# Performance work log

Hardware: AMD Instinct MI355X
Metric: run time of the kernel (lower is better)

## Reference

```python
import jax, jax.numpy as jnp
import numpy as np

# PillarEncoder constants (KITTI PointPillars config)
VX, VY = 0.16, 0.16
PCR = (0.0, -39.68, -3.0, 69.12, 39.68, 1.0)
X_OFFSET = VX / 2 + PCR[0]          # 0.08
Y_OFFSET = VY / 2 + PCR[1]          # -39.60
X_GRID = int((PCR[3] - PCR[0]) / VX)  # 432
Y_GRID = int((PCR[4] - PCR[1]) / VY)  # 496
C_OUT = 64
BN_EPS = 1e-5


def _bn(x, g, b, m, v):
    # inference-mode BatchNorm over the last (channel) axis
    return (x - m) * (g / jnp.sqrt(v + BN_EPS)) + b


def setup_inputs() -> dict:
    key = jax.random.key(0)
    ks = jax.random.split(key, 8)
    B, PPB, N = 4, 16000, 32
    P = B * PPB  # 64000 pillars total
    pillars = jax.random.normal(ks[0], (P, N, 4), dtype=jnp.float32)
    # scale xyz into the point-cloud range roughly
    scale = jnp.array([20.0, 15.0, 1.0, 0.3], dtype=jnp.float32)
    shift = jnp.array([35.0, 0.0, -1.0, 0.5], dtype=jnp.float32)
    pillars = pillars * scale + shift
    bidx = jnp.repeat(jnp.arange(B, dtype=jnp.int64), PPB)
    xidx = jax.random.randint(ks[1], (P,), 0, X_GRID, dtype=jnp.int64)
    yidx = jax.random.randint(ks[2], (P,), 0, Y_GRID, dtype=jnp.int64)
    coors_batch = jnp.stack([bidx, xidx, yidx, jnp.zeros((P,), jnp.int64)], axis=1)
    npoints_per_pillar = jax.random.randint(ks[3], (P,), 1, N + 1, dtype=jnp.int64)
    W1 = jax.random.normal(ks[4], (C_OUT, 6), dtype=jnp.float32) * 0.3
    W2 = jax.random.normal(ks[5], (C_OUT, C_OUT), dtype=jnp.float32) * 0.1
    ones = jnp.ones((C_OUT,), jnp.float32)
    zeros = jnp.zeros((C_OUT,), jnp.float32)
    return {
        'pillars': pillars, 'coors_batch': coors_batch,
        'npoints_per_pillar': npoints_per_pillar, 'batch_size': 4,
        'W1': W1, 'g1': ones, 'b1': zeros, 'm1': zeros, 'v1': ones,
        'W2': W2, 'g2': ones, 'b2': zeros, 'm2': zeros, 'v2': ones,
    }


def reference(pillars, coors_batch, npoints_per_pillar, batch_size,
              W1, g1, b1, m1, v1, W2, g2, b2, m2, v2):
    P, N, _ = pillars.shape
    npf = npoints_per_pillar.astype(pillars.dtype)
    # offset from per-pillar point-cloud mean (xyz)
    center = jnp.sum(pillars[:, :, :3], axis=1, keepdims=True) / npf[:, None, None]
    offset_pt_center = pillars[:, :, :3] - center  # (P,N,3)
    # offset from pillar geometric center
    px = coors_batch[:, None, 1:2].astype(pillars.dtype) * VX + X_OFFSET
    py = coors_batch[:, None, 2:3].astype(pillars.dtype) * VY + Y_OFFSET
    x_off = pillars[:, :, 0:1] - px
    y_off = pillars[:, :, 1:2] - py
    features = jnp.concatenate(
        [pillars[:, :, 2:3], offset_pt_center, x_off, y_off], axis=-1)  # (P,N,6)
    # mask padded points
    mask = (jnp.arange(N)[None, :] < npoints_per_pillar[:, None])
    features = features * mask[:, :, None].astype(features.dtype)
    # pointwise MLP: Conv1d(k=1) == per-point linear; BN in inference mode
    h = jnp.einsum('pnc,oc->pno', features, W1)
    h = jax.nn.relu(_bn(h, g1, b1, m1, v1))
    h = jnp.einsum('pnc,oc->pno', h, W2)
    h = _bn(h, g2, b2, m2, v2)
    pooled = jnp.max(h, axis=1)  # (P, C_OUT)
    # matching torch advanced-index assignment)
    flat = (coors_batch[:, 0] * (X_GRID * Y_GRID)
            + coors_batch[:, 1] * Y_GRID + coors_batch[:, 2])
    canvas = jnp.zeros((batch_size * X_GRID * Y_GRID, C_OUT), pooled.dtype)
    canvas = canvas.at[flat].set(pooled)
    canvas = canvas.reshape(batch_size, X_GRID, Y_GRID, C_OUT)
    # torch: canvas.permute(2,1,0) -> (C, y_grid, x_grid); batched -> (B,C,Y,X)
    pseudo_image = jnp.transpose(canvas, (0, 3, 2, 1))
    return pseudo_image
```

## Files before the change

kernel.cpp:

```cpp
#include <hip/hip_runtime.h>
#include <math.h>

#define XG 432
#define YG 496
#define NPTS 32
#define COUT 64
#define ROWH 72
#define TILE 64

typedef __attribute__((ext_vector_type(8))) __bf16 bf16x8;
typedef __attribute__((ext_vector_type(16))) float f32x16;

union ABFrag { bf16x8 v; unsigned short s[8]; };

__device__ __forceinline__ unsigned short f2bf(float f) {
    unsigned u = __builtin_bit_cast(unsigned, f);
    u = (u + 0x7fffu + ((u >> 16) & 1u)) >> 16;
    return (unsigned short)u;
}

__global__ __launch_bounds__(256) void precompute_kernel(
    const float* __restrict__ W1,
    const float* __restrict__ g1, const float* __restrict__ b1,
    const float* __restrict__ m1, const float* __restrict__ v1,
    const float* __restrict__ W2,
    const float* __restrict__ g2, const float* __restrict__ b2,
    const float* __restrict__ m2, const float* __restrict__ v2,
    unsigned short* __restrict__ w1f,
    unsigned short* __restrict__ w2f,
    float* __restrict__ bnp)
{
    const int t = threadIdx.x;
    if (t < 128) {
        const int tt = t >> 6, lane = t & 63;
        const int half = lane >> 5, l31 = lane & 31;
        unsigned short vals[8] = {0,0,0,0,0,0,0,0};
        if (half == 0) {
            const int co = tt * 32 + l31;
            for (int k = 0; k < 6; ++k) vals[k] = f2bf(W1[co * 6 + k]);
        }
        for (int j = 0; j < 8; ++j) w1f[(tt * 64 + lane) * 8 + j] = vals[j];
    }
    if (t < 64) {
        const float s1 = g1[t] * rsqrtf(v1[t] + 1e-5f);
        bnp[t]       = s1;
        bnp[64 + t]  = b1[t] - m1[t] * s1;
        const float s2 = g2[t] * rsqrtf(v2[t] + 1e-5f);
        bnp[128 + t] = s2;
        bnp[192 + t] = b2[t] - m2[t] * s2;
    }
    for (int idx = t; idx < 512; idx += 256) {
        const int tt   = idx >> 8;
        const int kt   = (idx >> 6) & 3;
        const int lane = idx & 63;
        const int half = lane >> 5, l31 = lane & 31;
        const int co = tt * 32 + l31;
        for (int j = 0; j < 8; ++j) {
            const int kp = kt * 16 + half * 8 + j;
            const int ci = ((kp & 1) << 5) | (kp >> 1);
            w2f[((tt * 4 + kt) * 64 + lane) * 8 + j] = f2bf(W2[co * COUT + ci]);
        }
    }
}

__global__ __launch_bounds__(256) void pillar_mlp_kernel(
    const float* __restrict__ pillars,
    const int*   __restrict__ coors,
    const int*   __restrict__ npp,
    const unsigned short* __restrict__ w1f,
    const unsigned short* __restrict__ w2f,
    const float* __restrict__ bnp,
    float* __restrict__ pooled,
    int*   __restrict__ winner,
    int P)
{
    __shared__ unsigned int sh1[4][NPTS * (ROWH / 2)];

    const int w    = threadIdx.x >> 6;
    const int lane = threadIdx.x & 63;
    const int half = lane >> 5;
    const int l31  = lane & 31;
    const int p    = blockIdx.x * 4 + w;
    const int pc   = (p < P) ? p : (P - 1);

    const bf16x8* w2v = (const bf16x8*)w2f;
    bf16x8 b2f[8];
    #pragma unroll
    for (int i = 0; i < 8; ++i) b2f[i] = w2v[i * 64 + lane];
    const bf16x8* w1v = (const bf16x8*)w1f;
    const bf16x8 b1f0 = w1v[lane];
    const bf16x8 b1f1 = w1v[64 + lane];

    float s1a[2], bb1a[2], s2a[2], bb2a[2];
    #pragma unroll
    for (int t = 0; t < 2; ++t) {
        const int co = t * 32 + l31;
        s1a[t]  = bnp[co];
        bb1a[t] = bnp[64 + co];
        s2a[t]  = bnp[128 + co];
        bb2a[t] = bnp[192 + co];
    }

    float4 pt = make_float4(0.f, 0.f, 0.f, 0.f);
    if (lane < NPTS) pt = ((const float4*)pillars)[(size_t)pc * NPTS + lane];
    float sx = pt.x, sy = pt.y, sz = pt.z;
    #pragma unroll
    for (int m = 1; m <= 16; m <<= 1) {
        sx += __shfl_xor(sx, m);
        sy += __shfl_xor(sy, m);
        sz += __shfl_xor(sz, m);
    }
    const int   np     = npp[pc];
    const float inv_np = 1.0f / (float)np;
    const float cx = sx * inv_np, cy = sy * inv_np, cz = sz * inv_np;

    const int cb  = coors[pc * 4 + 0];
    const int cxg = coors[pc * 4 + 1];
    const int cyg = coors[pc * 4 + 2];
    const float px = (float)cxg * 0.16f + 0.08f;
    const float py = (float)cyg * 0.16f + (-39.60f);

    ABFrag a1;
    #pragma unroll
    for (int j = 0; j < 8; ++j) a1.s[j] = 0;
    if (lane < np) {
        a1.s[0] = f2bf(pt.z);
        a1.s[1] = f2bf(pt.x - cx);
        a1.s[2] = f2bf(pt.y - cy);
        a1.s[3] = f2bf(pt.z - cz);
        a1.s[4] = f2bf(pt.x - px);
        a1.s[5] = f2bf(pt.y - py);
    }

    f32x16 d0, d1;
    #pragma unroll
    for (int i = 0; i < 16; ++i) { d0[i] = 0.f; d1[i] = 0.f; }
    d0 = __builtin_amdgcn_mfma_f32_32x32x16_bf16(a1.v, b1f0, d0, 0, 0, 0);
    d1 = __builtin_amdgcn_mfma_f32_32x32x16_bf16(a1.v, b1f1, d1, 0, 0, 0);

    unsigned int* row = sh1[w];
    #pragma unroll
    for (int r = 0; r < 16; ++r) {
        const int point = (r & 3) + 8 * (r >> 2) + 4 * half;
        const float h0 = fmaxf(d0[r] * s1a[0] + bb1a[0], 0.f);
        const float h1 = fmaxf(d1[r] * s1a[1] + bb1a[1], 0.f);
        const unsigned pk = (unsigned)f2bf(h0) | ((unsigned)f2bf(h1) << 16);
        row[point * (ROWH / 2) + l31] = pk;
    }

    const unsigned short* rowh = (const unsigned short*)sh1[w];
    bf16x8 a2[4];
    #pragma unroll
    for (int kt = 0; kt < 4; ++kt)
        a2[kt] = *(const bf16x8*)(rowh + l31 * ROWH + kt * 16 + half * 8);

    f32x16 c0, c1;
    #pragma unroll
    for (int i = 0; i < 16; ++i) { c0[i] = 0.f; c1[i] = 0.f; }
    #pragma unroll
    for (int kt = 0; kt < 4; ++kt) {
        c0 = __builtin_amdgcn_mfma_f32_32x32x16_bf16(a2[kt], b2f[kt],     c0, 0, 0, 0);
        c1 = __builtin_amdgcn_mfma_f32_32x32x16_bf16(a2[kt], b2f[4 + kt], c1, 0, 0, 0);
    }

    float mx0 = -INFINITY, mx1 = -INFINITY;
    #pragma unroll
    for (int r = 0; r < 16; ++r) {
        mx0 = fmaxf(mx0, c0[r] * s2a[0] + bb2a[0]);
        mx1 = fmaxf(mx1, c1[r] * s2a[1] + bb2a[1]);
    }
    mx0 = fmaxf(mx0, __shfl_xor(mx0, 32));
    mx1 = fmaxf(mx1, __shfl_xor(mx1, 32));

    if (p < P) {
        pooled[(size_t)p * COUT + lane] = half ? mx1 : mx0;
        if (lane == 0)
            atomicMax(&winner[cb * (YG * XG) + cyg * XG + cxg], p);
    }
}

__global__ __launch_bounds__(256) void scatter_kernel(
    const float4* __restrict__ pooled4,
    const int*    __restrict__ winner,
    float4* __restrict__ out,
    int ntx)
{
    __shared__ int   swn[TILE];
    __shared__ float st[TILE * COUT];

    const int bid  = blockIdx.x;
    const int tx   = bid % ntx;
    const int rest = bid / ntx;
    const int y    = rest % YG;
    const int b    = rest / YG;
    const int x0   = tx * TILE;
    const int tid  = threadIdx.x;

    if (tid < TILE) {
        const int x = x0 + tid;
        swn[tid] = (x < XG) ? winner[(b * YG + y) * XG + x] : -1;
    }
    __syncthreads();

    float4* st4 = (float4*)st;
    #pragma unroll
    for (int i = 0; i < 4; ++i) {
        const int f    = i * 256 + tid;
        const int cell = f >> 4, q = f & 15;
        const int wn   = swn[cell];
        float4 v = make_float4(0.f, 0.f, 0.f, 0.f);
        if (wn >= 0) v = pooled4[(size_t)wn * 16 + q];
        const int qp = q ^ (((cell >> 2) ^ cell) & 15);
        st4[cell * 16 + qp] = v;
    }
    __syncthreads();

    #pragma unroll
    for (int i = 0; i < 4; ++i) {
        const int f   = i * 256 + tid;
        const int ch  = f >> 4, xi4 = f & 15;
        const int x   = x0 + xi4 * 4;
        if (x >= XG) continue;
        const int g = ch >> 2, cl = ch & 3;
        float vals[4];
        #pragma unroll
        for (int r = 0; r < 4; ++r) {
            const int cell = xi4 * 4 + r;
            const int gp = g ^ (((cell >> 2) ^ cell) & 15);
            vals[r] = st[cell * COUT + gp * 4 + cl];
        }
        out[((size_t)(b * COUT + ch) * YG + y) * (XG / 4) + (x >> 2)] =
            make_float4(vals[0], vals[1], vals[2], vals[3]);
    }
}

extern "C" void kernel_launch(void* const* d_in, const int* in_sizes, int n_in,
                              void* d_out, int out_size, void* d_ws, size_t ws_size,
                              hipStream_t stream) {
    const float* pillars = (const float*)d_in[0];
    const int*   coors   = (const int*)d_in[1];
    const int*   npp     = (const int*)d_in[2];
    const float* W1 = (const float*)d_in[4];
    const float* g1 = (const float*)d_in[5];
    const float* b1 = (const float*)d_in[6];
    const float* m1 = (const float*)d_in[7];
    const float* v1 = (const float*)d_in[8];
    const float* W2 = (const float*)d_in[9];
    const float* g2 = (const float*)d_in[10];
    const float* b2 = (const float*)d_in[11];
    const float* m2 = (const float*)d_in[12];
    const float* v2 = (const float*)d_in[13];

    const int P = in_sizes[2];
    const int B = out_size / (COUT * YG * XG);

    float* pooled = (float*)d_ws;
    int*   winner = (int*)((char*)d_ws + (size_t)COUT * P * sizeof(float));

    char* fragbase = (char*)d_out + (size_t)out_size * sizeof(float) - 11264;
    unsigned short* w1f = (unsigned short*)fragbase;
    unsigned short* w2f = (unsigned short*)(fragbase + 2048);
    float*          bnp = (float*)(fragbase + 10240);

    precompute_kernel<<<1, 256, 0, stream>>>(
        W1, g1, b1, m1, v1, W2, g2, b2, m2, v2, w1f, w2f, bnp);

    (void)hipMemsetAsync(winner, 0xFF, (size_t)B * YG * XG * sizeof(int), stream);

    pillar_mlp_kernel<<<(P + 3) / 4, 256, 0, stream>>>(
        pillars, coors, npp, w1f, w2f, bnp, pooled, winner, P);

    const int ntx = (XG + TILE - 1) / TILE;
    scatter_kernel<<<B * YG * ntx, 256, 0, stream>>>(
        (const float4*)pooled, winner, (float4*)d_out, ntx);
}
```

Before: 347.5 us.

## Fold BatchNorm into MLP weights, pack bf16 in hardware, use nontemporal output stores

The BN scales are folded into the bf16 W1/W2 fragments, and the BN1 bias rides along as a constant-one input column in the first MFMA. Only the BN2 bias is added, once, after the max-pool. This removes per-element scale/bias arithmetic from the MLP kernel. The ReLU output is packed with the hardware cvt_pk_bf16 instruction when available, and the scatter kernel writes the large pseudo-image with nontemporal stores to reduce cache pollution. Folding weights and bias into bf16 adds some rounding error compared with applying BN in fp32.

```diff
diff --git a/kernel.cpp b/kernel.cpp
--- a/kernel.cpp
+++ b/kernel.cpp
@@ -9,7 +9,9 @@
 #define TILE 64
 
 typedef __attribute__((ext_vector_type(8))) __bf16 bf16x8;
+typedef __attribute__((ext_vector_type(2))) __bf16 bf16x2;
 typedef __attribute__((ext_vector_type(16))) float f32x16;
+typedef __attribute__((ext_vector_type(4))) float f32x4;
 
 union ABFrag { bf16x8 v; unsigned short s[8]; };
 
@@ -17,6 +19,15 @@
     unsigned u = __builtin_bit_cast(unsigned, f);
     u = (u + 0x7fffu + ((u >> 16) & 1u)) >> 16;
     return (unsigned short)u;
+}
+
+__device__ __forceinline__ unsigned pack_bf16(float a, float b) {
+#if __has_builtin(__builtin_amdgcn_cvt_pk_bf16_f32)
+    bf16x2 r = __builtin_amdgcn_cvt_pk_bf16_f32(a, b);
+    return __builtin_bit_cast(unsigned, r);
+#else
+    return (unsigned)f2bf(a) | ((unsigned)f2bf(b) << 16);
+#endif
 }
 
 __global__ __launch_bounds__(256) void precompute_kernel(
@@ -28,7 +39,7 @@
     const float* __restrict__ m2, const float* __restrict__ v2,
     unsigned short* __restrict__ w1f,
     unsigned short* __restrict__ w2f,
-    float* __restrict__ bnp)
+    float* __restrict__ bb2v)
 {
     const int t = threadIdx.x;
     if (t < 128) {
@@ -37,17 +48,16 @@
         unsigned short vals[8] = {0,0,0,0,0,0,0,0};
         if (half == 0) {
             const int co = tt * 32 + l31;
-            for (int k = 0; k < 6; ++k) vals[k] = f2bf(W1[co * 6 + k]);
+            const float s1  = g1[co] * rsqrtf(v1[co] + 1e-5f);
+            const float bb1 = b1[co] - m1[co] * s1;
+            for (int k = 0; k < 6; ++k) vals[k] = f2bf(W1[co * 6 + k] * s1);
+            vals[6] = f2bf(bb1);
         }
         for (int j = 0; j < 8; ++j) w1f[(tt * 64 + lane) * 8 + j] = vals[j];
     }
     if (t < 64) {
-        const float s1 = g1[t] * rsqrtf(v1[t] + 1e-5f);
-        bnp[t]       = s1;
-        bnp[64 + t]  = b1[t] - m1[t] * s1;
         const float s2 = g2[t] * rsqrtf(v2[t] + 1e-5f);
-        bnp[128 + t] = s2;
-        bnp[192 + t] = b2[t] - m2[t] * s2;
+        bb2v[t] = b2[t] - m2[t] * s2;
     }
     for (int idx = t; idx < 512; idx += 256) {
         const int tt   = idx >> 8;
@@ -55,10 +65,11 @@
         const int lane = idx & 63;
         const int half = lane >> 5, l31 = lane & 31;
         const int co = tt * 32 + l31;
+        const float s2 = g2[co] * rsqrtf(v2[co] + 1e-5f);
         for (int j = 0; j < 8; ++j) {
             const int kp = kt * 16 + half * 8 + j;
             const int ci = ((kp & 1) << 5) | (kp >> 1);
-            w2f[((tt * 4 + kt) * 64 + lane) * 8 + j] = f2bf(W2[co * COUT + ci]);
+            w2f[((tt * 4 + kt) * 64 + lane) * 8 + j] = f2bf(W2[co * COUT + ci] * s2);
         }
     }
 }
@@ -69,7 +80,7 @@
     const int*   __restrict__ npp,
     const unsigned short* __restrict__ w1f,
     const unsigned short* __restrict__ w2f,
-    const float* __restrict__ bnp,
+    const float* __restrict__ bb2v,
     float* __restrict__ pooled,
     int*   __restrict__ winner,
     int P)
@@ -90,16 +101,7 @@
     const bf16x8* w1v = (const bf16x8*)w1f;
     const bf16x8 b1f0 = w1v[lane];
     const bf16x8 b1f1 = w1v[64 + lane];
-
-    float s1a[2], bb1a[2], s2a[2], bb2a[2];
-    #pragma unroll
-    for (int t = 0; t < 2; ++t) {
-        const int co = t * 32 + l31;
-        s1a[t]  = bnp[co];
-        bb1a[t] = bnp[64 + co];
-        s2a[t]  = bnp[128 + co];
-        bb2a[t] = bnp[192 + co];
-    }
+    const float bb2 = bb2v[lane];
 
     float4 pt = make_float4(0.f, 0.f, 0.f, 0.f);
     if (lane < NPTS) pt = ((const float4*)pillars)[(size_t)pc * NPTS + lane];
@@ -123,6 +125,7 @@
     ABFrag a1;
     #pragma unroll
     for (int j = 0; j < 8; ++j) a1.s[j] = 0;
+    if (half == 0) a1.s[6] = 0x3F80;
     if (lane < np) {
         a1.s[0] = f2bf(pt.z);
         a1.s[1] = f2bf(pt.x - cx);
@@ -142,10 +145,8 @@
     #pragma unroll
     for (int r = 0; r < 16; ++r) {
         const int point = (r & 3) + 8 * (r >> 2) + 4 * half;
-        const float h0 = fmaxf(d0[r] * s1a[0] + bb1a[0], 0.f);
-        const float h1 = fmaxf(d1[r] * s1a[1] + bb1a[1], 0.f);
-        const unsigned pk = (unsigned)f2bf(h0) | ((unsigned)f2bf(h1) << 16);
-        row[point * (ROWH / 2) + l31] = pk;
+        row[point * (ROWH / 2) + l31] =
+            pack_bf16(fmaxf(d0[r], 0.f), fmaxf(d1[r], 0.f));
     }
 
     const unsigned short* rowh = (const unsigned short*)sh1[w];
@@ -166,14 +167,14 @@
     float mx0 = -INFINITY, mx1 = -INFINITY;
     #pragma unroll
     for (int r = 0; r < 16; ++r) {
-        mx0 = fmaxf(mx0, c0[r] * s2a[0] + bb2a[0]);
-        mx1 = fmaxf(mx1, c1[r] * s2a[1] + bb2a[1]);
+        mx0 = fmaxf(mx0, c0[r]);
+        mx1 = fmaxf(mx1, c1[r]);
     }
     mx0 = fmaxf(mx0, __shfl_xor(mx0, 32));
     mx1 = fmaxf(mx1, __shfl_xor(mx1, 32));
 
     if (p < P) {
-        pooled[(size_t)p * COUT + lane] = half ? mx1 : mx0;
+        pooled[(size_t)p * COUT + lane] = (half ? mx1 : mx0) + bb2;
         if (lane == 0)
             atomicMax(&winner[cb * (YG * XG) + cyg * XG + cxg], p);
     }
@@ -182,7 +183,7 @@
 __global__ __launch_bounds__(256) void scatter_kernel(
     const float4* __restrict__ pooled4,
     const int*    __restrict__ winner,
-    float4* __restrict__ out,
+    f32x4* __restrict__ out,
     int ntx)
 {
     __shared__ int   swn[TILE];
@@ -222,15 +223,15 @@
         const int x   = x0 + xi4 * 4;
         if (x >= XG) continue;
         const int g = ch >> 2, cl = ch & 3;
-        float vals[4];
+        f32x4 vals;
         #pragma unroll
         for (int r = 0; r < 4; ++r) {
             const int cell = xi4 * 4 + r;
             const int gp = g ^ (((cell >> 2) ^ cell) & 15);
             vals[r] = st[cell * COUT + gp * 4 + cl];
         }
-        out[((size_t)(b * COUT + ch) * YG + y) * (XG / 4) + (x >> 2)] =
-            make_float4(vals[0], vals[1], vals[2], vals[3]);
+        __builtin_nontemporal_store(vals,
+            &out[((size_t)(b * COUT + ch) * YG + y) * (XG / 4) + (x >> 2)]);
     }
 }
 
@@ -258,19 +259,19 @@
     int*   winner = (int*)((char*)d_ws + (size_t)COUT * P * sizeof(float));
 
     char* fragbase = (char*)d_out + (size_t)out_size * sizeof(float) - 11264;
-    unsigned short* w1f = (unsigned short*)fragbase;
-    unsigned short* w2f = (unsigned short*)(fragbase + 2048);
-    float*          bnp = (float*)(fragbase + 10240);
+    unsigned short* w1f  = (unsigned short*)fragbase;
+    unsigned short* w2f  = (unsigned short*)(fragbase + 2048);
+    float*          bb2v = (float*)(fragbase + 10240);
 
     precompute_kernel<<<1, 256, 0, stream>>>(
-        W1, g1, b1, m1, v1, W2, g2, b2, m2, v2, w1f, w2f, bnp);
+        W1, g1, b1, m1, v1, W2, g2, b2, m2, v2, w1f, w2f, bb2v);
 
     (void)hipMemsetAsync(winner, 0xFF, (size_t)B * YG * XG * sizeof(int), stream);
 
     pillar_mlp_kernel<<<(P + 3) / 4, 256, 0, stream>>>(
-        pillars, coors, npp, w1f, w2f, bnp, pooled, winner, P);
+        pillars, coors, npp, w1f, w2f, bb2v, pooled, winner, P);
 
     const int ntx = (XG + TILE - 1) / TILE;
     scatter_kernel<<<B * YG * ntx, 256, 0, stream>>>(
-        (const float4*)pooled, winner, (float4*)d_out, ntx);
-}
+        (const float4*)pooled, winner, (f32x4*)d_out, ntx);
+}
```

Result: faster. 315.2 us (-9.3%).
